# Optimization experiments

Measured on AMD Instinct MI355X. Metric: run time of the kernel, lower is better.

Reference implementation:

```python
import jax, jax.numpy as jnp
import numpy as np

B_TRIALS = 64   # n_trials
DZ = 512        # latent / network dim
DU = 16         # input dim
DX = 256        # observation dim
T = 1000        # time steps
DECAY = 0.9
G = np.sqrt(2.0)


def setup_inputs() -> dict:
    key = jax.random.key(0)
    k0, k1, k2, k3, k4 = jax.random.split(key, 5)
    z0 = jax.random.normal(k0, (B_TRIALS, DZ), jnp.float32)
    v = jax.random.normal(k1, (B_TRIALS, DU, T), jnp.float32)
    # W ~ (1-decay) * g / sqrt(dz) * N(0,1), per Transition_FullRank init
    W = ((1.0 - DECAY) * G / np.sqrt(DZ)) * jax.random.normal(k2, (DZ, DZ), jnp.float32)
    # Wu: uniform init scaled by 1/sqrt(du)
    Wu = (jax.random.uniform(k3, (DZ, DU), jnp.float32) * 2.0 - 1.0) / np.sqrt(DU)
    h = jnp.zeros((DZ,), jnp.float32)
    # decay_param = log(-log(decay))
    decay_param = jnp.full((1,), np.log(-np.log(DECAY)), jnp.float32)
    # Affine_observation: B ~ sqrt(2/(dz+dv)) * N(0,1), dv=0
    B_obs = np.sqrt(2.0 / DZ) * jax.random.normal(k4, (DZ, DX), jnp.float32)
    Bias = jnp.zeros((DX,), jnp.float32)
    return dict(z0=z0, v=v, W=W, Wu=Wu, h=h, decay_param=decay_param,
                B_obs=B_obs, Bias=Bias)


def reference(z0, v, W, Wu, h, decay_param, B_obs, Bias):
    # decay = exp(-exp(decay_param))
    decay = jnp.exp(-jnp.exp(decay_param[0]))
    v_seq = jnp.transpose(v, (2, 0, 1))  # [T, B, du]

    def step(z, vt):
        # z' = decay*z + W @ relu(z - h) + Wu @ v_t  (per trial)
        z_new = decay * z + jax.nn.relu(z - h) @ W.T + vt @ Wu.T
        return z_new, z_new

    _, zs = jax.lax.scan(step, z0, v_seq)      # [T, B, dz]
    zs = jnp.transpose(zs, (1, 2, 0))          # [B, dz, T]
    # Affine_observation (identity nonlinearity): einsum('zx,bzt->bxt') + bias
    x = jnp.einsum('zx,bzt->bxt', B_obs, zs) + Bias[None, :, None]
    return x
```

## Files before the change

kernel.cpp:

```cpp
#include <hip/hip_runtime.h>

#define DZc 512
#define Bc  64
#define Tc  1000
#define DUc 16
#define DXc 256
#define AROW 552


typedef __attribute__((ext_vector_type(4))) float f32x4;
typedef __attribute__((ext_vector_type(8))) short s16x8;
typedef __attribute__((ext_vector_type(4))) unsigned u32x4;

__device__ __forceinline__ unsigned short f2bf(float x) {
  unsigned u = __builtin_bit_cast(unsigned, x);
  u = u + 0x7FFFu + ((u >> 16) & 1u);
  return (unsigned short)(u >> 16);
}
__device__ __forceinline__ float bf2f(unsigned short u) {
  unsigned x = ((unsigned)u) << 16;
  return __builtin_bit_cast(float, x);
}
__device__ __forceinline__ unsigned cvt_pk_bf16(float lo, float hi) {
  unsigned r;
  asm("v_cvt_pk_bf16_f32 %0, %1, %2" : "=v"(r) : "v"(lo), "v"(hi));
  return r;
}
__device__ __forceinline__ float dpp_swap1(float x) {
  int r = __builtin_amdgcn_mov_dpp(__builtin_bit_cast(int, x), 0xB1, 0xF, 0xF, true);
  return __builtin_bit_cast(float, r);
}

__global__ void pack_w_kernel(const float* __restrict__ W,
                              const float* __restrict__ Wu,
                              unsigned short* __restrict__ Wp) {
  int d = blockIdx.x * 256 + threadIdx.x;
  int j = d & 7, l = (d >> 3) & 63, nt = (d >> 9) & 31, kt = d >> 14;
  int n = nt * 16 + (l & 15);
  int k = kt * 32 + ((l >> 4) << 3) + j;
  float val = (k < DZc) ? W[n * DZc + k] : Wu[n * DUc + (k & 15)];
  Wp[d] = f2bf(val);
}

__global__ void pack_b_kernel(const float* __restrict__ B,
                              unsigned short* __restrict__ Bp) {
  int d = blockIdx.x * 256 + threadIdx.x;
  int j = d & 7, l = (d >> 3) & 63, nt = (d >> 9) & 15, kt = d >> 13;
  int n = nt * 16 + (l & 15);
  int k = kt * 32 + ((l >> 4) << 3) + j;
  Bp[d] = f2bf(B[k * DXc + n]);
}

__global__ __launch_bounds__(512, 2) void rnn_rec_kernel(
    const float* __restrict__ z0, const float* __restrict__ v,
    const float* __restrict__ h, const float* __restrict__ dp,
    const unsigned short* __restrict__ Wp, unsigned short* __restrict__ zs,
    unsigned int* __restrict__ cnts) {
  __shared__ __align__(16) unsigned short abuf[2][16][AROW];
  __shared__ unsigned mode_sh;

  const int bid = blockIdx.x;
  const int g = bid & 7;
  const int s = bid >> 3;
  if (g >= 4) return;
  const int tid = threadIdx.x;
  const int lane = tid & 63;
  const int w = tid >> 6;
  const int l15 = lane & 15;
  const int lg = lane >> 4;
  const int b0 = g * 16;
  const int nbase = s * 256 + w * 32;

  unsigned int* mycnt = cnts + (g * 2 + s) * 16;
  const unsigned int* pcnt = cnts + (g * 2 + (s ^ 1)) * 16;

  if (tid == 0) {
    unsigned x;
    asm volatile("s_getreg_b32 %0, hwreg(HW_REG_XCC_ID)" : "=s"(x));
    x &= 0xFu;
    __hip_atomic_store(mycnt + 1, x | 0x10u, __ATOMIC_RELAXED,
                       __HIP_MEMORY_SCOPE_AGENT);
    unsigned px; int it = 0;
    do {
      px = __hip_atomic_load(pcnt + 1, __ATOMIC_RELAXED,
                             __HIP_MEMORY_SCOPE_AGENT);
    } while (!(px & 0x10u) && ++it < (1 << 20));
    mode_sh = ((px & 0x10u) && ((px & 0xFu) == x)) ? 1u : 0u;
  }

  s16x8 wr[34];
#pragma unroll
  for (int kt = 0; kt < 17; ++kt) {
#pragma unroll
    for (int ntl = 0; ntl < 2; ++ntl) {
      int nt = s * 16 + w * 2 + ntl;
      wr[kt * 2 + ntl] =
          *(const s16x8*)(Wp + ((size_t)((kt * 32 + nt) * 64 + lane)) * 8);
    }
  }

  float hreg[2];
  f32x4 acc[2];
#pragma unroll
  for (int ntl = 0; ntl < 2; ++ntl) {
    hreg[ntl] = h[nbase + ntl * 16 + l15];
#pragma unroll
    for (int r = 0; r < 4; ++r)
      acc[ntl][r] = z0[(size_t)(b0 + lg * 4 + r) * DZc + nbase + ntl * 16 + l15];
  }
  const float decay = expf(-expf(dp[0]));

  const int ptrial = tid >> 5;
  const int koff = (tid & 31) * 8;
  const int pk = (1 - s) * 256 + koff;
  float hpart[8];
#pragma unroll
  for (int j = 0; j < 8; ++j) hpart[j] = h[pk + j];

  const int du = tid & 15, trr = tid >> 4;
  const size_t vbase = ((size_t)(b0 + trr) * DUc + du) * Tc;
  float vcur = (tid < 256) ? v[vbase] : 0.f;

#pragma unroll
  for (int half = 0; half < 2; ++half) {
    int kk = half * 256 + koff;
    const float* zp = z0 + (size_t)(b0 + ptrial) * DZc + kk;
    s16x8 ov;
#pragma unroll
    for (int j = 0; j < 8; ++j) {
      float av = zp[j] - h[kk + j];
      ov[j] = (short)f2bf(av > 0.f ? av : 0.f);
    }
    *(s16x8*)&abuf[0][ptrial][kk] = ov;
  }
  if (tid < 256) {
    unsigned short hi = f2bf(vcur);
    abuf[0][trr][512 + du] = hi;
    abuf[0][trr][528 + du] = f2bf(vcur - bf2f(hi));
  }
  asm volatile("s_waitcnt lgkmcnt(0)\n\ts_barrier" ::: "memory");
  const bool fast = (mode_sh != 0);

  unsigned* zs32 = (unsigned*)zs;

  int p = 0;
  for (int t = 0; t < Tc; ++t) {
    float vnext = (tid < 256) ? v[vbase + (t + 1 < Tc ? t + 1 : Tc - 1)] : 0.f;
#pragma unroll
    for (int ntl = 0; ntl < 2; ++ntl)
#pragma unroll
      for (int r = 0; r < 4; ++r) acc[ntl][r] *= decay;

    if (t > 0) {
      int iters = 0;
      while (__hip_atomic_load(pcnt, __ATOMIC_RELAXED,
                               __HIP_MEMORY_SCOPE_AGENT) < (unsigned)t) {
        __builtin_amdgcn_s_sleep(2);
        if (++iters > (1 << 22)) break;
      }
      asm volatile("" ::: "memory");
      u32x4 pz4 = *(const u32x4*)(zs32 +
            ((size_t)(t - 1) * Bc + b0 + ptrial) * 256 + (pk >> 1));
      u32x4 av;
#pragma unroll
      for (int j2 = 0; j2 < 4; ++j2) {
        unsigned wd = pz4[j2];
        float lo = __builtin_bit_cast(float, wd << 16);
        float hi = __builtin_bit_cast(float, wd & 0xFFFF0000u);
        lo = lo - hpart[j2 * 2];
        hi = hi - hpart[j2 * 2 + 1];
        lo = lo > 0.f ? lo : 0.f;
        hi = hi > 0.f ? hi : 0.f;
        av[j2] = cvt_pk_bf16(lo, hi);
      }
      *(u32x4*)&abuf[p][ptrial][pk] = av;
    }

    asm volatile("s_waitcnt lgkmcnt(0)\n\ts_barrier" ::: "memory");

#pragma unroll
    for (int kt = 0; kt < 17; ++kt) {
      s16x8 af = *(const s16x8*)&abuf[p][l15][kt * 32 + lg * 8];
      acc[0] = __builtin_amdgcn_mfma_f32_16x16x32_bf16(af, wr[kt * 2 + 0], acc[0], 0, 0, 0);
      acc[1] = __builtin_amdgcn_mfma_f32_16x16x32_bf16(af, wr[kt * 2 + 1], acc[1], 0, 0, 0);
    }

    const size_t zrow0 = (size_t)t * Bc + b0 + lg * 4;
#pragma unroll
    for (int r = 0; r < 4; ++r) {
      float d0 = dpp_swap1(acc[0][r]);
      float d1 = dpp_swap1(acc[1][r]);
      if (!(lane & 1)) {
        unsigned c0 = cvt_pk_bf16(acc[0][r], d0);
        unsigned c1 = cvt_pk_bf16(acc[1][r], d1);
        unsigned* dst = zs32 + (zrow0 + r) * 256 + (nbase >> 1) + (l15 >> 1);
        if (fast) {
          dst[0] = c0;
          dst[8] = c1;
        } else {
          __hip_atomic_store(dst, c0, __ATOMIC_RELAXED, __HIP_MEMORY_SCOPE_AGENT);
          __hip_atomic_store(dst + 8, c1, __ATOMIC_RELAXED, __HIP_MEMORY_SCOPE_AGENT);
        }
      }
    }

    asm volatile("s_waitcnt vmcnt(0)" ::: "memory");
    __builtin_amdgcn_s_barrier();
    if (tid == 0)
      __hip_atomic_store(mycnt, (unsigned)(t + 1), __ATOMIC_RELAXED,
                         __HIP_MEMORY_SCOPE_AGENT);

#pragma unroll
    for (int r = 0; r < 4; ++r) {
      float a0 = acc[0][r] - hreg[0]; a0 = a0 > 0.f ? a0 : 0.f;
      float a1 = acc[1][r] - hreg[1]; a1 = a1 > 0.f ? a1 : 0.f;
      float d0 = dpp_swap1(a0);
      float d1 = dpp_swap1(a1);
      if (!(lane & 1)) {
        unsigned c0 = cvt_pk_bf16(a0, d0);
        unsigned c1 = cvt_pk_bf16(a1, d1);
        *(unsigned*)&abuf[p ^ 1][lg * 4 + r][nbase + (l15 & ~1)] = c0;
        *(unsigned*)&abuf[p ^ 1][lg * 4 + r][nbase + 16 + (l15 & ~1)] = c1;
      }
    }
    if (tid < 256) {
      unsigned short hi = f2bf(vnext);
      abuf[p ^ 1][trr][512 + du] = hi;
      abuf[p ^ 1][trr][528 + du] = f2bf(vnext - bf2f(hi));
    }

    p ^= 1;
    vcur = vnext;
  }
}

__global__ __launch_bounds__(256, 1) void rnn_proj_kernel(
    const unsigned short* __restrict__ zs, const unsigned short* __restrict__ Bp,
    const float* __restrict__ Bias, float* __restrict__ x) {
  const int wg = blockIdx.x;
  const int b = wg / 63;
  const int tbase = (wg % 63) * 16;
  const int tid = threadIdx.x;
  const int lane = tid & 63;
  const int w = tid >> 6;
  const int l15 = lane & 15, lg = lane >> 4;

  const int trow = tbase + l15;
  const int trc = trow < Tc ? trow : Tc - 1;
  const unsigned short* abase = zs + ((size_t)trc * Bc + b) * DZc + lg * 8;
  const s16x8 zz = {0, 0, 0, 0, 0, 0, 0, 0};

  f32x4 acc[4];
#pragma unroll
  for (int n = 0; n < 4; ++n)
#pragma unroll
    for (int e = 0; e < 4; ++e) acc[n][e] = 0.f;

#pragma unroll
  for (int kt = 0; kt < 16; ++kt) {
    s16x8 af = *(const s16x8*)(abase + kt * 32);
    af = (trow < Tc) ? af : zz;
#pragma unroll
    for (int n = 0; n < 4; ++n) {
      s16x8 bf = *(const s16x8*)(Bp + (size_t)((kt * 16 + w * 4 + n) * 64 + lane) * 8);
      acc[n] = __builtin_amdgcn_mfma_f32_16x16x32_bf16(af, bf, acc[n], 0, 0, 0);
    }
  }

  const int t = tbase + lg * 4;
  if (t < Tc) {
#pragma unroll
    for (int n = 0; n < 4; ++n) {
      int xo = (w * 4 + n) * 16 + l15;
      float bias = Bias[xo];
      f32x4 val = acc[n];
#pragma unroll
      for (int e = 0; e < 4; ++e) val[e] += bias;
      *(f32x4*)(x + ((size_t)b * DXc + xo) * Tc + t) = val;
    }
  }
}

extern "C" void kernel_launch(void* const* d_in, const int* in_sizes, int n_in,
                              void* d_out, int out_size, void* d_ws, size_t ws_size,
                              hipStream_t stream) {
  const float* z0   = (const float*)d_in[0];
  const float* v    = (const float*)d_in[1];
  const float* W    = (const float*)d_in[2];
  const float* Wu   = (const float*)d_in[3];
  const float* h    = (const float*)d_in[4];
  const float* dp   = (const float*)d_in[5];
  const float* Bo   = (const float*)d_in[6];
  const float* Bias = (const float*)d_in[7];
  float* x = (float*)d_out;

  unsigned short* Wp = (unsigned short*)d_ws;
  unsigned short* Bp = Wp + 278528;
  unsigned short* zs = Bp + 131072;
  unsigned int* cnts = (unsigned int*)(zs + 32768000);

  hipMemsetAsync(cnts, 0, 128 * sizeof(unsigned int), stream);
  pack_w_kernel<<<1088, 256, 0, stream>>>(W, Wu, Wp);
  pack_b_kernel<<<512, 256, 0, stream>>>(Bo, Bp);
  rnn_rec_kernel<<<16, 512, 0, stream>>>(z0, v, h, dp, Wp, zs, cnts);
  rnn_proj_kernel<<<4032, 256, 0, stream>>>(zs, Bp, Bias, x);
}
```

Measured before the change: 1.954 ms.

## Launch extra blocks and pair recurrence blocks dynamically by XCC id

The recurrence kernel now launches 64 blocks. Each block registers its XCC id in a global table, and once all 64 have registered they deterministically pick four pairs of blocks that share an XCC. Paired blocks on the same XCC can use the fast cross-block handshake path instead of falling back to slow mode. This replaces the fixed pairing, which only ran fast when the hardware happened to co-locate the pair. In exchange it adds a grid-wide registration spin-wait and relies on all 64 blocks being co-resident.

```diff
diff --git a/kernel.cpp b/kernel.cpp
--- a/kernel.cpp
+++ b/kernel.cpp
@@ -57,13 +57,74 @@
     const unsigned short* __restrict__ Wp, unsigned short* __restrict__ zs,
     unsigned int* __restrict__ cnts) {
   __shared__ __align__(16) unsigned short abuf[2][16][AROW];
-  __shared__ unsigned mode_sh;
+  __shared__ unsigned role_sh;
 
   const int bid = blockIdx.x;
-  const int g = bid & 7;
-  const int s = bid >> 3;
-  if (g >= 4) return;
   const int tid = threadIdx.x;
+
+  unsigned int* regtab = cnts + 128;
+  unsigned int* regcnt = cnts + 192;
+
+  if (tid == 0) {
+    unsigned x;
+    asm volatile("s_getreg_b32 %0, hwreg(HW_REG_XCC_ID)" : "=s"(x));
+    x &= 0xFu;
+    __hip_atomic_store(&regtab[bid], x | 0x100u, __ATOMIC_RELAXED,
+                       __HIP_MEMORY_SCOPE_AGENT);
+    __hip_atomic_fetch_add(regcnt, 1u, __ATOMIC_RELAXED,
+                           __HIP_MEMORY_SCOPE_AGENT);
+    int it = 0;
+    while (__hip_atomic_load(regcnt, __ATOMIC_RELAXED,
+                             __HIP_MEMORY_SCOPE_AGENT) < 64u &&
+           ++it < (1 << 24))
+      __builtin_amdgcn_s_sleep(1);
+    unsigned tab[64];
+    for (int i = 0; i < 64; ++i)
+      tab[i] = __hip_atomic_load(&regtab[i], __ATOMIC_RELAXED,
+                                 __HIP_MEMORY_SCOPE_AGENT);
+    unsigned used[64];
+    for (int i = 0; i < 64; ++i) used[i] = 0;
+    int pg = -1, ps = -1, fm = 0, pairs = 0;
+    for (int xc = 0; xc < 16 && pairs < 4; ++xc) {
+      int first = -1;
+      for (int i = 0; i < 64 && pairs < 4; ++i) {
+        if (!(tab[i] & 0x100u) || used[i] || (int)(tab[i] & 0xFu) != xc)
+          continue;
+        if (first < 0) { first = i; }
+        else {
+          if (bid == first) { pg = pairs; ps = 0; fm = 1; }
+          if (bid == i)     { pg = pairs; ps = 1; fm = 1; }
+          used[first] = used[i] = 1;
+          ++pairs;
+          first = -1;
+        }
+      }
+    }
+    while (pairs < 4) {
+      int a = -1, b = -1;
+      for (int i = 0; i < 64; ++i) {
+        if (used[i] || !(tab[i] & 0x100u)) continue;
+        if (a < 0) a = i;
+        else { b = i; break; }
+      }
+      if (a < 0) a = pairs * 2;
+      if (b < 0) b = pairs * 2 + 1;
+      if (bid == a) { pg = pairs; ps = 0; fm = 0; }
+      if (bid == b) { pg = pairs; ps = 1; fm = 0; }
+      if (a < 64) used[a] = 1;
+      if (b < 64) used[b] = 1;
+      ++pairs;
+    }
+    role_sh = (pg < 0) ? 0xFFFFFFFFu
+              : ((unsigned)pg | ((unsigned)ps << 8) | ((unsigned)fm << 16));
+  }
+  __syncthreads();
+  const unsigned role = role_sh;
+  if (role == 0xFFFFFFFFu) return;
+  const int g = role & 0xFF;
+  const int s = (role >> 8) & 0xFF;
+  const bool fast = ((role >> 16) & 1) != 0;
+
   const int lane = tid & 63;
   const int w = tid >> 6;
   const int l15 = lane & 15;
@@ -74,20 +135,6 @@
   unsigned int* mycnt = cnts + (g * 2 + s) * 16;
   const unsigned int* pcnt = cnts + (g * 2 + (s ^ 1)) * 16;
 
-  if (tid == 0) {
-    unsigned x;
-    asm volatile("s_getreg_b32 %0, hwreg(HW_REG_XCC_ID)" : "=s"(x));
-    x &= 0xFu;
-    __hip_atomic_store(mycnt + 1, x | 0x10u, __ATOMIC_RELAXED,
-                       __HIP_MEMORY_SCOPE_AGENT);
-    unsigned px; int it = 0;
-    do {
-      px = __hip_atomic_load(pcnt + 1, __ATOMIC_RELAXED,
-                             __HIP_MEMORY_SCOPE_AGENT);
-    } while (!(px & 0x10u) && ++it < (1 << 20));
-    mode_sh = ((px & 0x10u) && ((px & 0xFu) == x)) ? 1u : 0u;
-  }
-
   s16x8 wr[34];
 #pragma unroll
   for (int kt = 0; kt < 17; ++kt) {
@@ -139,7 +186,6 @@
     abuf[0][trr][528 + du] = f2bf(vcur - bf2f(hi));
   }
   asm volatile("s_waitcnt lgkmcnt(0)\n\ts_barrier" ::: "memory");
-  const bool fast = (mode_sh != 0);
 
   unsigned* zs32 = (unsigned*)zs;
 
@@ -299,9 +345,9 @@
   unsigned short* zs = Bp + 131072;
   unsigned int* cnts = (unsigned int*)(zs + 32768000);
 
-  hipMemsetAsync(cnts, 0, 128 * sizeof(unsigned int), stream);
+  hipMemsetAsync(cnts, 0, 256 * sizeof(unsigned int), stream);
   pack_w_kernel<<<1088, 256, 0, stream>>>(W, Wu, Wp);
   pack_b_kernel<<<512, 256, 0, stream>>>(Bo, Bp);
-  rnn_rec_kernel<<<16, 512, 0, stream>>>(z0, v, h, dp, Wp, zs, cnts);
+  rnn_rec_kernel<<<64, 512, 0, stream>>>(z0, v, h, dp, Wp, zs, cnts);
   rnn_proj_kernel<<<4032, 256, 0, stream>>>(zs, Bp, Bias, x);
 }
```

After: 2.050 ms. 4.9% more time.
